# Kernel tuning notes

Measured on AMD Instinct MI355X. Metric: run time of the kernel, lower is better.

Reference implementation:

```python
import jax, jax.numpy as jnp
import numpy as np
import itertools

# ---- model dimensions ----
NELEC = 10   # total electrons
NSPIN = 2    # spin_split = 2 -> equal split (5, 5)
NPER = 5     # electrons per spin block
D = 3        # spatial dimension
NION = 2     # number of ions (diatomic)
DP = 32      # backflow output feature dim d'
NDENSE = 64  # ndense_resnet


def _perms_and_signs(n):
    perms = np.array(list(itertools.permutations(range(n))), dtype=np.int32)
    signs = np.empty(len(perms), dtype=np.float32)
    for i, p in enumerate(perms):
        inv = sum(1 for a in range(n) for b in range(a + 1, n) if p[a] > p[b])
        signs[i] = -1.0 if inv % 2 else 1.0
    return jnp.asarray(perms), jnp.asarray(signs)

# constant permutation indices/signs (closed over; not differentiated)
PERMS, SIGNS = _perms_and_signs(NPER)  # (120, 5), (120,)


def setup_inputs() -> dict:
    key = jax.random.key(0)
    ks = jax.random.split(key, 8)
    B = 2048
    feat = NION * D + NION  # backflow input features per electron: r_ei flat + |r_ei|
    nin = NPER * DP         # flattened spin-block input to each ResNet
    return {
        "elec_pos": jax.random.normal(ks[0], (B, NELEC, D), jnp.float32),
        "ion_pos": jax.random.normal(ks[1], (NION, D), jnp.float32) * 2.0,
        "bf_w": jax.random.normal(ks[2], (feat, DP), jnp.float32) / np.sqrt(feat),
        "bf_b": jnp.zeros((DP,), jnp.float32),
        "w0": jax.random.normal(ks[3], (NSPIN, nin, NDENSE), jnp.float32) / np.sqrt(nin),
        "b0": jnp.zeros((NSPIN, NDENSE), jnp.float32),
        "w1": jax.random.normal(ks[4], (NSPIN, NDENSE, NDENSE), jnp.float32) / np.sqrt(NDENSE),
        "b1": jnp.zeros((NSPIN, NDENSE), jnp.float32),
        "w2": jax.random.normal(ks[5], (NSPIN, NDENSE, 1), jnp.float32) / np.sqrt(NDENSE),
        "b2": jnp.zeros((NSPIN, 1), jnp.float32),
        "jastrow_kernel": jnp.ones((NION,), jnp.float32),
    }


def _spin_antisym(block, W0, B0, W1, B1, W2, B2):
    # block: (B, NPER, DP) one spin block of the 1e stream
    B = block.shape[0]
    xp = block[:, PERMS, :]                  # (B, nperm, NPER, DP) all permutations
    xp = xp.reshape(B, PERMS.shape[0], NPER * DP)
    # SimpleResNet: dense->act, residual middle layer, final linear to 1
    h = jnp.tanh(xp @ W0 + B0)
    h = jnp.tanh(h @ W1 + B1) + h            # residual (shapes match)
    out = (h @ W2 + B2)[..., 0]              # (B, nperm)
    return jnp.sum(out * SIGNS, axis=-1)     # signed perm-sum -> (B,)


def reference(elec_pos, ion_pos, bf_w, bf_b, w0, b0, w1, b1, w2, b2, jastrow_kernel):
    B = elec_pos.shape[0]
    # backflow: r_ei features -> dense -> tanh
    r_ei = elec_pos[..., :, None, :] - ion_pos          # (B, nelec, nion, d)
    r_norm = jnp.linalg.norm(r_ei, axis=-1)             # (B, nelec, nion)
    feats = jnp.concatenate([r_ei.reshape(B, NELEC, NION * D), r_norm], axis=-1)
    stream_1e = jnp.tanh(feats @ bf_w + bf_b)           # (B, nelec, DP)
    # split into equal spin blocks (spin_split=2)
    blocks = jnp.stack(jnp.split(stream_1e, NSPIN, axis=-2), axis=0)  # (NSPIN, B, NPER, DP)
    per_spin = jax.vmap(_spin_antisym)(blocks, w0, b0, w1, b1, w2, b2)  # (NSPIN, B)
    antisymmetric_part = jnp.log(jnp.abs(jnp.prod(per_spin, axis=0)))   # (B,)
    # isotropic atomic exponential decay jastrow (log domain)
    jastrow_part = -jnp.sum(jastrow_kernel * r_norm, axis=(-1, -2))     # (B,)
    return antisymmetric_part + jastrow_part
```

## Files before the change

kernel.cpp:

```cpp
#include <hip/hip_runtime.h>
#include <math.h>

#define NELEC 10
#define NSPIN 2
#define NPER 5
#define DIM 3
#define NION 2
#define DP 32
#define NDENSE 64
#define NPERM 120
#define RS 324
#define HTS 124

#define POOL_WORDS (NDENSE * HTS)

typedef float v2f __attribute__((ext_vector_type(2)));
typedef float v4f __attribute__((ext_vector_type(4)));

#define PK_FMA_LO(acc, hp, wp) \
    asm("v_pk_fma_f32 %0, %1, %2, %0 op_sel_hi:[1,0,1]" : "+v"(acc) : "v"(hp), "v"(wp))
#define PK_FMA_HI(acc, hp, wp) \
    asm("v_pk_fma_f32 %0, %1, %2, %0 op_sel:[0,1,0] op_sel_hi:[1,1,1]" : "+v"(acc) : "v"(hp), "v"(wp))

__device__ __forceinline__ float fast_tanh(float x) {
    float e = __expf(2.0f * x);
    return 1.0f - 2.0f * __builtin_amdgcn_rcpf(e + 1.0f);
}

__device__ __forceinline__ unsigned pick_remove(unsigned& el, int d) {
    unsigned v = (el >> (4 * d)) & 0xFu;
    unsigned low = el & ((1u << (4 * d)) - 1u);
    el = low | ((el >> (4 * (d + 1))) << (4 * d));
    return v;
}

__global__ __launch_bounds__(128, 1) void antisym_kern(
    const float* __restrict__ elec_pos, const float* __restrict__ ion_pos,
    const float* __restrict__ bf_w, const float* __restrict__ bf_b,
    const float* __restrict__ w0, const float* __restrict__ b0,
    const float* __restrict__ w1, const float* __restrict__ b1,
    const float* __restrict__ w2,
    float* __restrict__ psum, int B)
{
    const int b = blockIdx.x;
    const int s = blockIdx.y;
    const int t = threadIdx.x;
    const int wave = t >> 6, lane = t & 63;

    __shared__ __align__(16) float pool[POOL_WORDS];
    __shared__ double red_h[2];
    __shared__ double red_j[2];

    float* s1e = pool;
    #define GROW(j) (pool + 160 + (j) * RS)
    #define HTROW(k) (pool + (k) * HTS)

    const float* ep = elec_pos + (b * NELEC + s * NPER) * DIM;
    const float i0x = ion_pos[0], i0y = ion_pos[1], i0z = ion_pos[2];
    const float i1x = ion_pos[3], i1y = ion_pos[4], i1z = ion_pos[5];
    for (int idx = t; idx < NPER * DP; idx += 128) {
        int j = idx >> 5, c = idx & 31;
        float ex = ep[j * 3 + 0], ey = ep[j * 3 + 1], ez = ep[j * 3 + 2];
        float dx0 = ex - i0x, dy0 = ey - i0y, dz0 = ez - i0z;
        float dx1 = ex - i1x, dy1 = ey - i1y, dz1 = ez - i1z;
        float n0 = sqrtf(dx0 * dx0 + dy0 * dy0 + dz0 * dz0);
        float n1 = sqrtf(dx1 * dx1 + dy1 * dy1 + dz1 * dz1);
        float acc = bf_b[c];
        acc += dx0 * bf_w[0 * DP + c];
        acc += dy0 * bf_w[1 * DP + c];
        acc += dz0 * bf_w[2 * DP + c];
        acc += dx1 * bf_w[3 * DP + c];
        acc += dy1 * bf_w[4 * DP + c];
        acc += dz1 * bf_w[5 * DP + c];
        acc += n0 * bf_w[6 * DP + c];
        acc += n1 * bf_w[7 * DP + c];
        s1e[idx] = fast_tanh(acc);
    }
    __syncthreads();

    const float* w0s = w0 + s * (NPER * DP) * NDENSE;
    for (int j = wave; j < NPER; j += 2) {
        float4 sv4[8];
        #pragma unroll
        for (int q = 0; q < 8; q++) sv4[q] = *(const float4*)(s1e + j * DP + q * 4);
        #pragma unroll
        for (int i = 0; i < NPER; i++) {
            float acc = 0.f;
            #pragma unroll
            for (int q = 0; q < 8; q++) {
                const float* wb = w0s + (i * DP + q * 4) * NDENSE + lane;
                acc += sv4[q].x * wb[0 * NDENSE];
                acc += sv4[q].y * wb[1 * NDENSE];
                acc += sv4[q].z * wb[2 * NDENSE];
                acc += sv4[q].w * wb[3 * NDENSE];
            }
            GROW(j)[i * NDENSE + lane] = acc;
        }
    }
    __syncthreads();

    const float* b0s = b0 + s * NDENSE;
    const float* w2s = w2 + s * NDENSE;

    const int pid = wave * 60 + lane;
    float sign = 0.f;
    int p0 = 0, p1 = 0, p2 = 0, p3 = 0, p4 = 0;
    if (lane < 60) {
        int p = pid;
        unsigned el = 0x43210u;
        int d0 = p / 24; p -= d0 * 24;
        int d1 = p / 6;  p -= d1 * 6;
        int d2 = p / 2;  p -= d2 * 2;
        int d3 = p;
        p0 = pick_remove(el, d0);
        p1 = pick_remove(el, d1);
        p2 = pick_remove(el, d2);
        p3 = pick_remove(el, d3);
        p4 = el & 0xF;
        sign = ((d0 + d1 + d2 + d3) & 1) ? -1.f : 1.f;
    }
    const float* g0 = GROW(p0) + 0 * NDENSE;
    const float* g1 = GROW(p1) + 1 * NDENSE;
    const float* g2 = GROW(p2) + 2 * NDENSE;
    const float* g3 = GROW(p3) + 3 * NDENSE;
    const float* g4 = GROW(p4) + 4 * NDENSE;

    float h[NDENSE];
    float hdot = 0.f;
    #pragma unroll
    for (int cc = 0; cc < NDENSE / 4; cc++) {
        float4 a = *(const float4*)(b0s + cc * 4);
        float4 q;
        q = *(const float4*)(g0 + cc * 4); a.x += q.x; a.y += q.y; a.z += q.z; a.w += q.w;
        q = *(const float4*)(g1 + cc * 4); a.x += q.x; a.y += q.y; a.z += q.z; a.w += q.w;
        q = *(const float4*)(g2 + cc * 4); a.x += q.x; a.y += q.y; a.z += q.z; a.w += q.w;
        q = *(const float4*)(g3 + cc * 4); a.x += q.x; a.y += q.y; a.z += q.z; a.w += q.w;
        q = *(const float4*)(g4 + cc * 4); a.x += q.x; a.y += q.y; a.z += q.z; a.w += q.w;
        float t0 = fast_tanh(a.x), t1 = fast_tanh(a.y), t2 = fast_tanh(a.z), t3 = fast_tanh(a.w);
        h[cc * 4 + 0] = t0; h[cc * 4 + 1] = t1; h[cc * 4 + 2] = t2; h[cc * 4 + 3] = t3;
        hdot += t0 * w2s[cc * 4 + 0] + t1 * w2s[cc * 4 + 1]
              + t2 * w2s[cc * 4 + 2] + t3 * w2s[cc * 4 + 3];
    }

    double dvh = (double)(sign * hdot);
    #pragma unroll
    for (int off = 32; off > 0; off >>= 1) dvh += __shfl_down(dvh, off, 64);
    if (lane == 0) red_h[wave] = dvh;

    __syncthreads();

    if (lane < 60) {
        #pragma unroll
        for (int k = 0; k < NDENSE; k++) HTROW(k)[pid] = h[k];
    }
    __syncthreads();

    const int pg = lane >> 3, jg = lane & 7;
    const int pb = wave ? (56 + 8 * pg) : (8 * pg);
    const float* w1s = w1 + s * NDENSE * NDENSE;
    const float* b1s = b1 + s * NDENSE;
    const float* wgp = w1s + 8 * jg;

    v2f vp[4][8];
    #pragma unroll
    for (int ip = 0; ip < 4; ip++)
        #pragma unroll
        for (int r = 0; r < 8; r++) vp[ip][r] = (v2f)(0.f);

    v4f ha_n = *(const v4f*)(&HTROW(0)[pb]);
    v4f hb_n = *(const v4f*)(&HTROW(0)[pb + 4]);
    v4f wa_n = *(const v4f*)(wgp);
    v4f wb_n = *(const v4f*)(wgp + 4);
    #pragma unroll 4
    for (int k = 0; k < NDENSE; k++) {
        const v4f ha = ha_n, hb = hb_n, wa = wa_n, wb = wb_n;
        if (k + 1 < NDENSE) {
            ha_n = *(const v4f*)(&HTROW(k + 1)[pb]);
            hb_n = *(const v4f*)(&HTROW(k + 1)[pb + 4]);
            wa_n = *(const v4f*)(wgp + (k + 1) * NDENSE);
            wb_n = *(const v4f*)(wgp + (k + 1) * NDENSE + 4);
        }
        v2f hp[4] = {ha.xy, ha.zw, hb.xy, hb.zw};
        v2f wp[4] = {wa.xy, wa.zw, wb.xy, wb.zw};
        #pragma unroll
        for (int ip = 0; ip < 4; ip++) {
            PK_FMA_LO(vp[ip][0], hp[ip], wp[0]);
            PK_FMA_HI(vp[ip][1], hp[ip], wp[0]);
            PK_FMA_LO(vp[ip][2], hp[ip], wp[1]);
            PK_FMA_HI(vp[ip][3], hp[ip], wp[1]);
            PK_FMA_LO(vp[ip][4], hp[ip], wp[2]);
            PK_FMA_HI(vp[ip][5], hp[ip], wp[2]);
            PK_FMA_LO(vp[ip][6], hp[ip], wp[3]);
            PK_FMA_HI(vp[ip][7], hp[ip], wp[3]);
        }
    }

    float4 b1a = *(const float4*)(b1s + 8 * jg);
    float4 b1b = *(const float4*)(b1s + 8 * jg + 4);
    float4 w2a = *(const float4*)(w2s + 8 * jg);
    float4 w2b = *(const float4*)(w2s + 8 * jg + 4);
    const float b1v[8] = {b1a.x, b1a.y, b1a.z, b1a.w, b1b.x, b1b.y, b1b.z, b1b.w};
    const float w2v[8] = {w2a.x, w2a.y, w2a.z, w2a.w, w2b.x, w2b.y, w2b.z, w2b.w};

    float lanesum = 0.f;
    #pragma unroll
    for (int i = 0; i < 8; i++) {
        int p = pb + i;
        int d0 = p / 24;  int r0 = p - 24 * d0;
        int d1 = r0 / 6;  int r1 = r0 - 6 * d1;
        int d2 = r1 >> 1; int d3 = r1 & 1;
        float sgn = ((d0 + d1 + d2 + d3) & 1) ? -1.f : 1.f;
        if (wave == 1 && pg == 0) sgn = 0.f;
        float si = 0.f;
        #pragma unroll
        for (int r = 0; r < 8; r++) {
            float vir = (i & 1) ? vp[i >> 1][r].y : vp[i >> 1][r].x;
            si = fmaf(fast_tanh(vir + b1v[r]), w2v[r], si);
        }
        lanesum = fmaf(sgn, si, lanesum);
    }

    double dvj = (double)lanesum;
    #pragma unroll
    for (int off = 32; off > 0; off >>= 1) dvj += __shfl_down(dvj, off, 64);
    if (lane == 0) red_j[wave] = dvj;
    __syncthreads();
    if (t == 0)
        psum[s * B + b] = (float)((red_h[0] + red_h[1]) + (red_j[0] + red_j[1]));
}

__global__ void combine_kern(const float* __restrict__ psum,
                             const float* __restrict__ elec_pos,
                             const float* __restrict__ ion_pos,
                             const float* __restrict__ jk,
                             float* __restrict__ out, int B)
{
    int b = blockIdx.x * 256 + threadIdx.x;
    if (b >= B) return;
    const float i0x = ion_pos[0], i0y = ion_pos[1], i0z = ion_pos[2];
    const float i1x = ion_pos[3], i1y = ion_pos[4], i1z = ion_pos[5];
    const float j0 = jk[0], j1 = jk[1];
    const float* ep = elec_pos + b * NELEC * DIM;
    float jas = 0.f;
    #pragma unroll
    for (int e = 0; e < NELEC; e++) {
        float ex = ep[e * 3 + 0], ey = ep[e * 3 + 1], ez = ep[e * 3 + 2];
        float dx0 = ex - i0x, dy0 = ey - i0y, dz0 = ez - i0z;
        float dx1 = ex - i1x, dy1 = ey - i1y, dz1 = ez - i1z;
        jas += j0 * sqrtf(dx0 * dx0 + dy0 * dy0 + dz0 * dz0);
        jas += j1 * sqrtf(dx1 * dx1 + dy1 * dy1 + dz1 * dz1);
    }
    float ps0 = psum[b], ps1 = psum[B + b];
    out[b] = logf(fabsf(ps0 * ps1)) - jas;
}

extern "C" void kernel_launch(void* const* d_in, const int* in_sizes, int n_in,
                              void* d_out, int out_size, void* d_ws, size_t ws_size,
                              hipStream_t stream) {
    const float* elec_pos = (const float*)d_in[0];
    const float* ion_pos  = (const float*)d_in[1];
    const float* bf_w     = (const float*)d_in[2];
    const float* bf_b     = (const float*)d_in[3];
    const float* w0       = (const float*)d_in[4];
    const float* b0       = (const float*)d_in[5];
    const float* w1       = (const float*)d_in[6];
    const float* b1       = (const float*)d_in[7];
    const float* w2       = (const float*)d_in[8];
    const float* jk       = (const float*)d_in[10];
    float* out = (float*)d_out;

    const int B = in_sizes[0] / (NELEC * DIM);

    float* psum = (float*)d_ws;

    hipLaunchKernelGGL(antisym_kern,
                       dim3(B, NSPIN), dim3(128), 0, stream,
                       elec_pos, ion_pos, bf_w, bf_b, w0, b0, w1, b1, w2, psum, B);
    hipLaunchKernelGGL(combine_kern,
                       dim3((B + 255) / 256), dim3(256), 0, stream,
                       psum, elec_pos, ion_pos, jk, out, B);
}
```

Baseline: 161.7 us.

## Fuse both spin blocks and the jastrow/log combine into one kernel

Merges the two spin-block workgroups into a single 256-thread block per batch element, each half handling one spin, and folds the jastrow and log-combine step into the end of that kernel. This drops the second kernel launch and the round trip of partial sums through global memory. In exchange it doubles shared memory per block (two pools of about 32 KB each) and halves the grid size. Block-wide barriers now couple both spins, so the two halves can no longer run independently.

```diff
diff --git a/kernel.cpp b/kernel.cpp
--- a/kernel.cpp
+++ b/kernel.cpp
@@ -34,31 +34,34 @@
     return v;
 }
 
-__global__ __launch_bounds__(128, 1) void antisym_kern(
+__global__ __launch_bounds__(256, 1) void antisym_fused(
     const float* __restrict__ elec_pos, const float* __restrict__ ion_pos,
     const float* __restrict__ bf_w, const float* __restrict__ bf_b,
     const float* __restrict__ w0, const float* __restrict__ b0,
     const float* __restrict__ w1, const float* __restrict__ b1,
-    const float* __restrict__ w2,
-    float* __restrict__ psum, int B)
+    const float* __restrict__ w2, const float* __restrict__ jk,
+    float* __restrict__ out, int B)
 {
     const int b = blockIdx.x;
-    const int s = blockIdx.y;
     const int t = threadIdx.x;
-    const int wave = t >> 6, lane = t & 63;
-
-    __shared__ __align__(16) float pool[POOL_WORDS];
-    __shared__ double red_h[2];
-    __shared__ double red_j[2];
-
-    float* s1e = pool;
-    #define GROW(j) (pool + 160 + (j) * RS)
-    #define HTROW(k) (pool + (k) * HTS)
+    const int s = t >> 7;
+    const int ts = t & 127;
+    const int wave = (t >> 6) & 1;
+    const int lane = t & 63;
+
+    __shared__ __align__(16) float pool[NSPIN][POOL_WORDS];
+    __shared__ double red_h[NSPIN][2];
+    __shared__ double red_j[NSPIN][2];
+    __shared__ float jterm[2 * NELEC];
+
+    float* s1e = pool[s];
+    #define GROW(j) (pool[s] + 160 + (j) * RS)
+    #define HTROW(k) (pool[s] + (k) * HTS)
 
     const float* ep = elec_pos + (b * NELEC + s * NPER) * DIM;
     const float i0x = ion_pos[0], i0y = ion_pos[1], i0z = ion_pos[2];
     const float i1x = ion_pos[3], i1y = ion_pos[4], i1z = ion_pos[5];
-    for (int idx = t; idx < NPER * DP; idx += 128) {
+    for (int idx = ts; idx < NPER * DP; idx += 128) {
         int j = idx >> 5, c = idx & 31;
         float ex = ep[j * 3 + 0], ey = ep[j * 3 + 1], ez = ep[j * 3 + 2];
         float dx0 = ex - i0x, dy0 = ey - i0y, dz0 = ez - i0z;
@@ -76,6 +79,14 @@
         acc += n1 * bf_w[7 * DP + c];
         s1e[idx] = fast_tanh(acc);
     }
+    if (t < 2 * NELEC) {
+        int e = t >> 1, ion = t & 1;
+        const float* epb = elec_pos + b * NELEC * DIM;
+        float ex = epb[e * 3 + 0], ey = epb[e * 3 + 1], ez = epb[e * 3 + 2];
+        float ix = ion_pos[ion * 3 + 0], iy = ion_pos[ion * 3 + 1], iz = ion_pos[ion * 3 + 2];
+        float dx = ex - ix, dy = ey - iy, dz = ez - iz;
+        jterm[t] = jk[ion] * sqrtf(dx * dx + dy * dy + dz * dz);
+    }
     __syncthreads();
 
     const float* w0s = w0 + s * (NPER * DP) * NDENSE;
@@ -145,7 +156,7 @@
     double dvh = (double)(sign * hdot);
     #pragma unroll
     for (int off = 32; off > 0; off >>= 1) dvh += __shfl_down(dvh, off, 64);
-    if (lane == 0) red_h[wave] = dvh;
+    if (lane == 0) red_h[s][wave] = dvh;
 
     __syncthreads();
 
@@ -223,35 +234,17 @@
     double dvj = (double)lanesum;
     #pragma unroll
     for (int off = 32; off > 0; off >>= 1) dvj += __shfl_down(dvj, off, 64);
-    if (lane == 0) red_j[wave] = dvj;
-    __syncthreads();
-    if (t == 0)
-        psum[s * B + b] = (float)((red_h[0] + red_h[1]) + (red_j[0] + red_j[1]));
-}
-
-__global__ void combine_kern(const float* __restrict__ psum,
-                             const float* __restrict__ elec_pos,
-                             const float* __restrict__ ion_pos,
-                             const float* __restrict__ jk,
-                             float* __restrict__ out, int B)
-{
-    int b = blockIdx.x * 256 + threadIdx.x;
-    if (b >= B) return;
-    const float i0x = ion_pos[0], i0y = ion_pos[1], i0z = ion_pos[2];
-    const float i1x = ion_pos[3], i1y = ion_pos[4], i1z = ion_pos[5];
-    const float j0 = jk[0], j1 = jk[1];
-    const float* ep = elec_pos + b * NELEC * DIM;
-    float jas = 0.f;
-    #pragma unroll
-    for (int e = 0; e < NELEC; e++) {
-        float ex = ep[e * 3 + 0], ey = ep[e * 3 + 1], ez = ep[e * 3 + 2];
-        float dx0 = ex - i0x, dy0 = ey - i0y, dz0 = ez - i0z;
-        float dx1 = ex - i1x, dy1 = ey - i1y, dz1 = ez - i1z;
-        jas += j0 * sqrtf(dx0 * dx0 + dy0 * dy0 + dz0 * dz0);
-        jas += j1 * sqrtf(dx1 * dx1 + dy1 * dy1 + dz1 * dz1);
-    }
-    float ps0 = psum[b], ps1 = psum[B + b];
-    out[b] = logf(fabsf(ps0 * ps1)) - jas;
+    if (lane == 0) red_j[s][wave] = dvj;
+    __syncthreads();
+
+    if (t == 0) {
+        float ps0 = (float)((red_h[0][0] + red_h[0][1]) + (red_j[0][0] + red_j[0][1]));
+        float ps1 = (float)((red_h[1][0] + red_h[1][1]) + (red_j[1][0] + red_j[1][1]));
+        float jas = 0.f;
+        #pragma unroll
+        for (int i = 0; i < 2 * NELEC; i++) jas += jterm[i];
+        out[b] = logf(fabsf(ps0 * ps1)) - jas;
+    }
 }
 
 extern "C" void kernel_launch(void* const* d_in, const int* in_sizes, int n_in,
@@ -271,12 +264,7 @@
 
     const int B = in_sizes[0] / (NELEC * DIM);
 
-    float* psum = (float*)d_ws;
-
-    hipLaunchKernelGGL(antisym_kern,
-                       dim3(B, NSPIN), dim3(128), 0, stream,
-                       elec_pos, ion_pos, bf_w, bf_b, w0, b0, w1, b1, w2, psum, B);
-    hipLaunchKernelGGL(combine_kern,
-                       dim3((B + 255) / 256), dim3(256), 0, stream,
-                       psum, elec_pos, ion_pos, jk, out, B);
-}
+    hipLaunchKernelGGL(antisym_fused,
+                       dim3(B), dim3(256), 0, stream,
+                       elec_pos, ion_pos, bf_w, bf_b, w0, b0, w1, b1, w2, jk, out, B);
+}
```

New measurement: 155.5 us. 3.8% less time.
